# Optimization experiments

Measured on AMD Instinct MI355X. Metric: run time of the kernel, lower is better.

Reference implementation:

```python
import jax, jax.numpy as jnp
import numpy as np

N0, N1, N2 = 120000, 30000, 6000   # node frontier sizes per hop
E0, E1 = 480000, 96000             # sampled edges per layer (~fanout 16)
D = 128                            # in_channels == hidden_size
R = 8                              # num_relations
NB = 4                             # num_bases
ETOT = 3000000                     # global edge count (edge_type_all)


def setup_inputs() -> dict:
    key = jax.random.key(0)
    ks = jax.random.split(key, 24)
    s = 1.0 / np.sqrt(D)
    f32 = jnp.float32
    inp = {
        "x": jax.random.normal(ks[0], (N0, D), dtype=f32),
        "src0": jax.random.randint(ks[1], (E0,), 0, N0),
        "dst0": jax.random.randint(ks[2], (E0,), 0, N1),
        "e_id0": jax.random.randint(ks[3], (E0,), 0, ETOT),
        "src1": jax.random.randint(ks[4], (E1,), 0, N1),
        "dst1": jax.random.randint(ks[5], (E1,), 0, N2),
        "e_id1": jax.random.randint(ks[6], (E1,), 0, ETOT),
        "edge_type_all": jax.random.randint(ks[7], (ETOT,), 0, R),
        # pre_layer: linear + relu
        "pre_W": jax.random.normal(ks[8], (D, D), dtype=f32) * s,
        "pre_b": jnp.zeros((D,), f32),
        # RGCNConv layer 0 (basis decomposition)
        "basis0": jax.random.normal(ks[9], (NB, D, D), dtype=f32) * s,
        "comp0": jax.random.normal(ks[10], (R, NB), dtype=f32) * (1.0 / np.sqrt(NB)),
        "root0": jax.random.normal(ks[11], (D, D), dtype=f32) * s,
        "bias0": jnp.zeros((D,), f32),
        "g0": jnp.ones((D,), f32),
        "be0": jnp.zeros((D,), f32),
        # RGCNConv layer 1
        "basis1": jax.random.normal(ks[12], (NB, D, D), dtype=f32) * s,
        "comp1": jax.random.normal(ks[13], (R, NB), dtype=f32) * (1.0 / np.sqrt(NB)),
        "root1": jax.random.normal(ks[14], (D, D), dtype=f32) * s,
        "bias1": jnp.zeros((D,), f32),
        "g1": jnp.ones((D,), f32),
        "be1": jnp.zeros((D,), f32),
        # post_layer: single linear
        "post_W": jax.random.normal(ks[15], (D, D), dtype=f32) * s,
        "post_b": jnp.zeros((D,), f32),
    }
    return inp


def _layernorm(x, g, b, eps=1e-5):
    mu = jnp.mean(x, axis=-1, keepdims=True)
    var = jnp.mean(jnp.square(x - mu), axis=-1, keepdims=True)
    return (x - mu) * jax.lax.rsqrt(var + eps) * g + b


def _rgcn_conv(x, n_dst, src, dst, etype, basis, comp, root, bias):
    # Bipartite RGCNConv with basis decomposition and mean aggregation.
    # Since messages W[r] @ x[src] are linear, aggregate per relation first
    # (segment_sum of raw features), then apply the relation weight once.
    x_t = x[:n_dst]                                    # [n_dst, D]
    out = x_t @ root + bias                            # root/self transform
    W = jnp.einsum('rb,bio->rio', comp, basis)         # [R, D, D]
    x_j = x[src]                                       # [E, D] gather
    deg = jax.ops.segment_sum(jnp.ones(src.shape[0], x.dtype), dst,
                              num_segments=n_dst)      # mean over all relations
    agg = jnp.zeros((n_dst, W.shape[-1]), x.dtype)
    for r in range(W.shape[0]):                        # R=8 structurally distinct
        m = (etype == r).astype(x.dtype)[:, None]
        s_r = jax.ops.segment_sum(x_j * m, dst, num_segments=n_dst)
        agg = agg + s_r @ W[r]
    return out + agg / jnp.maximum(deg, 1.0)[:, None]


def reference(x, src0, dst0, e_id0, src1, dst1, e_id1, edge_type_all,
              pre_W, pre_b, basis0, comp0, root0, bias0, g0, be0,
              basis1, comp1, root1, bias1, g1, be1, post_W, post_b):
    # pre_layer: linear + relu (GeneralMultiLayer, final_act=True)
    h = jax.nn.relu(x @ pre_W + pre_b)
    # layer 0: edge-type gather -> relational conv -> norm -> act (eval: no dropout)
    h = _rgcn_conv(h, N1, src0, dst0, edge_type_all[e_id0],
                   basis0, comp0, root0, bias0)
    h = jax.nn.relu(_layernorm(h, g0, be0))
    # layer 1
    h = _rgcn_conv(h, N2, src1, dst1, edge_type_all[e_id1],
                   basis1, comp1, root1, bias1)
    h = jax.nn.relu(_layernorm(h, g1, be1))
    # post_layer: single linear MLP
    return h @ post_W + post_b
```

## Files before the change

### kernel.cpp

```cpp
#include <hip/hip_runtime.h>
#include <cstdint>

#define DD 128
#define CAP 64
#define ESB 128
#define E0C 480000
#define E1C 96000
#define N0C 120000
#define N1C 30000
#define N2C 6000

typedef unsigned short u16;
typedef __attribute__((ext_vector_type(8))) short bf16x8;
typedef __attribute__((ext_vector_type(16))) float f32x16;

__device__ __forceinline__ u16 f2b(float f) {
    union { float f; unsigned u; } a; a.f = f;
    unsigned r = (a.u + 0x7fffu + ((a.u >> 16) & 1u)) >> 16;
    return (u16)r;
}
__device__ __forceinline__ float b2f(u16 u) {
    union { unsigned u; float f; } a; a.u = ((unsigned)u) << 16;
    return a.f;
}

struct WtJob { const float* src[12]; };
__global__ __launch_bounds__(256) void prep_kernel(
    WtJob job, u16* __restrict__ dst, int* __restrict__ cnt0, int* __restrict__ cnt1)
{
    int gtid = blockIdx.x * 256 + threadIdx.x;
    for (int i = gtid; i < N1C + N2C; i += 256 * 256) {
        if (i < N1C) cnt0[i] = 0; else cnt1[i - N1C] = 0;
    }
    if (blockIdx.x >= 192) return;
    __shared__ float tile[32][33];
    int m = blockIdx.x >> 4;
    int t4 = blockIdx.x & 15;
    int tr = (t4 >> 2) * 32;
    int tc = (t4 & 3) * 32;
    int lx = threadIdx.x & 31, ly = threadIdx.x >> 5;
    #pragma unroll
    for (int yy = 0; yy < 32; yy += 8)
        tile[ly + yy][lx] = job.src[m][(tr + ly + yy) * DD + tc + lx];
    __syncthreads();
    int tid = threadIdx.x;
    if (tid < 128) {
        int nl = tid >> 2, kch = tid & 3;
        int k = tr + kch * 8, n = tc + nl;
        int kc = k >> 4, half = (k >> 3) & 1;
        int t = n >> 5, l31 = n & 31;
        bf16x8 pk;
        #pragma unroll
        for (int j = 0; j < 8; ++j) pk[j] = (short)f2b(tile[kch * 8 + j][nl]);
        *(bf16x8*)(dst + (size_t)m * 16384 + kc * 2048 + t * 512 + half * 256 + l31 * 8) = pk;
    }
}

__global__ __launch_bounds__(256) void pre_fill_kernel(
    const float* __restrict__ x,
    const int* __restrict__ src0, const int* __restrict__ dst0, const int* __restrict__ eid0,
    const int* __restrict__ src1, const int* __restrict__ dst1, const int* __restrict__ eid1,
    const int* __restrict__ etype,
    int* __restrict__ cnt0, int* __restrict__ cnt1,
    int* __restrict__ ep0, int* __restrict__ ep1,
    const u16* __restrict__ Wr, const float* __restrict__ bias,
    u16* __restrict__ h0)
{
    if (blockIdx.x < ESB) {
        const int STR = ESB * 256;
        int gtid = blockIdx.x * 256 + threadIdx.x;
        int e = gtid;
        for (; e + 3 * STR < E0C + E1C; e += 4 * STR) {
            int d[4], eidv[4], s[4], r[4], pos[4];
            bool L0[4];
            #pragma unroll
            for (int u = 0; u < 4; ++u) {
                int idx = e + u * STR;
                L0[u] = idx < E0C;
                int ee = L0[u] ? idx : idx - E0C;
                d[u]    = L0[u] ? dst0[ee] : dst1[ee];
                eidv[u] = L0[u] ? eid0[ee] : eid1[ee];
                s[u]    = L0[u] ? src0[ee] : src1[ee];
            }
            #pragma unroll
            for (int u = 0; u < 4; ++u) r[u] = etype[eidv[u]];
            #pragma unroll
            for (int u = 0; u < 4; ++u)
                pos[u] = atomicAdd(L0[u] ? &cnt0[d[u]] : &cnt1[d[u]], 1);
            #pragma unroll
            for (int u = 0; u < 4; ++u) {
                if (pos[u] < CAP) {
                    int* ep = L0[u] ? ep0 : ep1;
                    ep[(size_t)d[u] * CAP + pos[u]] = s[u] | (r[u] << 28);
                }
            }
        }
        for (; e < E0C + E1C; e += STR) {
            bool L0 = e < E0C;
            int ee = L0 ? e : e - E0C;
            int d   = L0 ? dst0[ee] : dst1[ee];
            int eid = L0 ? eid0[ee] : eid1[ee];
            int s   = L0 ? src0[ee] : src1[ee];
            int r = etype[eid];
            int pos = atomicAdd(L0 ? &cnt0[d] : &cnt1[d], 1);
            if (pos < CAP) (L0 ? ep0 : ep1)[(size_t)d * CAP + pos] = s | (r << 28);
        }
        return;
    }

    int bid = blockIdx.x - ESB;
    int wave = threadIdx.x >> 6;
    int lane = threadIdx.x & 63;
    int l31 = lane & 31, half = lane >> 5;
    int m0 = (bid * 4 + wave) * 32;
    if (m0 >= N0C) return;
    int arow = m0 + l31;
    bool rv = arow < N0C;

    const float* Aq = x + (size_t)arow * DD;
    float4 st[16];
    if (rv) {
        #pragma unroll
        for (int c = 0; c < 16; ++c)
            st[c] = *(const float4*)(Aq + ((c >> 1) * 16 + half * 8) + (c & 1) * 4);
    } else {
        #pragma unroll
        for (int c = 0; c < 16; ++c) st[c] = make_float4(0.f, 0.f, 0.f, 0.f);
    }
    f32x16 accs[4];
    #pragma unroll
    for (int t = 0; t < 4; ++t)
        #pragma unroll
        for (int i = 0; i < 16; ++i) accs[t][i] = 0.f;
    #pragma unroll
    for (int kc = 0; kc < 8; ++kc) {
        bf16x8 bfr[4];
        #pragma unroll
        for (int t = 0; t < 4; ++t)
            bfr[t] = *(const bf16x8*)(Wr + (size_t)((kc * 4 + t) * 64 + lane) * 8);
        float4 u0 = st[2 * kc], u1 = st[2 * kc + 1];
        bf16x8 af;
        af[0] = (short)f2b(u0.x); af[1] = (short)f2b(u0.y);
        af[2] = (short)f2b(u0.z); af[3] = (short)f2b(u0.w);
        af[4] = (short)f2b(u1.x); af[5] = (short)f2b(u1.y);
        af[6] = (short)f2b(u1.z); af[7] = (short)f2b(u1.w);
        #pragma unroll
        for (int t = 0; t < 4; ++t)
            accs[t] = __builtin_amdgcn_mfma_f32_32x32x16_bf16(af, bfr[t], accs[t], 0, 0, 0);
    }
    float bb[4];
    #pragma unroll
    for (int t = 0; t < 4; ++t) bb[t] = bias[t * 32 + l31];
    #pragma unroll
    for (int reg = 0; reg < 16; ++reg) {
        int rl = (reg & 3) + 8 * (reg >> 2) + 4 * half;
        int row = m0 + rl;
        if (row < N0C) {
            #pragma unroll
            for (int t = 0; t < 4; ++t)
                h0[(size_t)row * DD + t * 32 + l31] =
                    f2b(fmaxf(accs[t][reg] + bb[t], 0.f));
        }
    }
}

__global__ __launch_bounds__(256) void agg_kernel(
    const u16* __restrict__ h, const int* __restrict__ cnt,
    const int* __restrict__ ep, const float* __restrict__ comp,
    u16* __restrict__ T, int ndst)
{
    __shared__ float4 cmp4[8];
    if (threadIdx.x < 8) cmp4[threadIdx.x] = ((const float4*)comp)[threadIdx.x];
    __syncthreads();
    int row = blockIdx.x * 4 + (threadIdx.x >> 6);
    if (row >= ndst) return;
    int lane = threadIdx.x & 63;
    int n = cnt[row];
    int end = n < CAP ? n : CAP;
    const int* erow = ep + (size_t)row * CAP;
    float a0[4] = {0.f, 0.f, 0.f, 0.f};
    float a1[4] = {0.f, 0.f, 0.f, 0.f};
    int j = 0;
    for (; j + 16 <= end; j += 16) {
        int vv[16]; unsigned gg[16];
        #pragma unroll
        for (int u = 0; u < 16; ++u) vv[u] = erow[j + u];
        #pragma unroll
        for (int u = 0; u < 16; ++u)
            gg[u] = *(const unsigned*)(h + (size_t)(vv[u] & 0x0FFFFFFF) * DD + 2 * lane);
        #pragma unroll
        for (int u = 0; u < 16; ++u) {
            float4 c = cmp4[vv[u] >> 28];
            float x0 = b2f((u16)(gg[u] & 0xffffu));
            float x1 = b2f((u16)(gg[u] >> 16));
            a0[0] = fmaf(c.x, x0, a0[0]); a1[0] = fmaf(c.x, x1, a1[0]);
            a0[1] = fmaf(c.y, x0, a0[1]); a1[1] = fmaf(c.y, x1, a1[1]);
            a0[2] = fmaf(c.z, x0, a0[2]); a1[2] = fmaf(c.z, x1, a1[2]);
            a0[3] = fmaf(c.w, x0, a0[3]); a1[3] = fmaf(c.w, x1, a1[3]);
        }
    }
    for (; j + 4 <= end; j += 4) {
        int vv[4]; unsigned gg[4];
        #pragma unroll
        for (int u = 0; u < 4; ++u) vv[u] = erow[j + u];
        #pragma unroll
        for (int u = 0; u < 4; ++u)
            gg[u] = *(const unsigned*)(h + (size_t)(vv[u] & 0x0FFFFFFF) * DD + 2 * lane);
        #pragma unroll
        for (int u = 0; u < 4; ++u) {
            float4 c = cmp4[vv[u] >> 28];
            float x0 = b2f((u16)(gg[u] & 0xffffu));
            float x1 = b2f((u16)(gg[u] >> 16));
            a0[0] = fmaf(c.x, x0, a0[0]); a1[0] = fmaf(c.x, x1, a1[0]);
            a0[1] = fmaf(c.y, x0, a0[1]); a1[1] = fmaf(c.y, x1, a1[1]);
            a0[2] = fmaf(c.z, x0, a0[2]); a1[2] = fmaf(c.z, x1, a1[2]);
            a0[3] = fmaf(c.w, x0, a0[3]); a1[3] = fmaf(c.w, x1, a1[3]);
        }
    }
    for (; j < end; ++j) {
        int v = erow[j];
        unsigned g = *(const unsigned*)(h + (size_t)(v & 0x0FFFFFFF) * DD + 2 * lane);
        float4 c = cmp4[v >> 28];
        float x0 = b2f((u16)(g & 0xffffu));
        float x1 = b2f((u16)(g >> 16));
        a0[0] = fmaf(c.x, x0, a0[0]); a1[0] = fmaf(c.x, x1, a1[0]);
        a0[1] = fmaf(c.y, x0, a0[1]); a1[1] = fmaf(c.y, x1, a1[1]);
        a0[2] = fmaf(c.z, x0, a0[2]); a1[2] = fmaf(c.z, x1, a1[2]);
        a0[3] = fmaf(c.w, x0, a0[3]); a1[3] = fmaf(c.w, x1, a1[3]);
    }
    float inv = 1.f / fmaxf((float)n, 1.f);
    #pragma unroll
    for (int b = 0; b < 4; ++b) {
        unsigned pk = (unsigned)f2b(a0[b] * inv) | ((unsigned)f2b(a1[b] * inv) << 16);
        *(unsigned*)(T + ((size_t)b * ndst + row) * DD + 2 * lane) = pk;
    }
}

template<bool OBF16, bool LN>
__global__ __launch_bounds__(64) void mfma_gemm(
    const u16* __restrict__ Ap, int nplanes, const u16* __restrict__ Ar,
    const u16* __restrict__ Wp, const u16* __restrict__ Wr,
    const float* __restrict__ bias, const float* __restrict__ gw,
    const float* __restrict__ bw, void* __restrict__ Cv, int nrows)
{
    int lane = threadIdx.x & 63;
    int l31 = lane & 31, half = lane >> 5;
    int m0 = blockIdx.x * 32;
    int arow = m0 + l31;
    bool rv = arow < nrows;
    f32x16 acc[4];
    #pragma unroll
    for (int t = 0; t < 4; ++t)
        #pragma unroll
        for (int i = 0; i < 16; ++i) acc[t][i] = 0.f;

    bf16x8 A0[8], A1[8];
    {
        const u16* Ainit = (nplanes == 0) ? Ar : Ap;
        if (rv) {
            #pragma unroll
            for (int c = 0; c < 8; ++c)
                A0[c] = *(const bf16x8*)(Ainit + (size_t)arow * DD + c * 16 + half * 8);
        } else {
            #pragma unroll
            for (int c = 0; c < 8; ++c) A0[c] = (bf16x8){0,0,0,0,0,0,0,0};
        }
    }
    for (int p = 0; p <= nplanes; ++p) {
        const u16* Wsel = (p == nplanes) ? Wr : Wp + p * 16384;
        if (p < nplanes) {
            const u16* An = (p + 1 == nplanes) ? Ar : Ap + (size_t)(p + 1) * nrows * DD;
            if (rv) {
                #pragma unroll
                for (int c = 0; c < 8; ++c)
                    A1[c] = *(const bf16x8*)(An + (size_t)arow * DD + c * 16 + half * 8);
            } else {
                #pragma unroll
                for (int c = 0; c < 8; ++c) A1[c] = (bf16x8){0,0,0,0,0,0,0,0};
            }
        }
        #pragma unroll
        for (int kc = 0; kc < 8; ++kc) {
            bf16x8 bfr[4];
            #pragma unroll
            for (int t = 0; t < 4; ++t)
                bfr[t] = *(const bf16x8*)(Wsel + (size_t)((kc * 4 + t) * 64 + lane) * 8);
            #pragma unroll
            for (int t = 0; t < 4; ++t)
                acc[t] = __builtin_amdgcn_mfma_f32_32x32x16_bf16(A0[kc], bfr[t], acc[t], 0, 0, 0);
        }
        if (p < nplanes) {
            #pragma unroll
            for (int c = 0; c < 8; ++c) A0[c] = A1[c];
        }
    }

    float bb[4];
    #pragma unroll
    for (int t = 0; t < 4; ++t) bb[t] = bias[t * 32 + l31];
    float gg[4], ww[4];
    if (LN) {
        #pragma unroll
        for (int t = 0; t < 4; ++t) { gg[t] = gw[t * 32 + l31]; ww[t] = bw[t * 32 + l31]; }
    }

    #pragma unroll
    for (int reg = 0; reg < 16; ++reg) {
        int rl = (reg & 3) + 8 * (reg >> 2) + 4 * half;
        int row = m0 + rl;
        float v[4];
        #pragma unroll
        for (int t = 0; t < 4; ++t) v[t] = acc[t][reg] + bb[t];
        if (LN) {
            float s1 = 0.f, s2 = 0.f;
            #pragma unroll
            for (int t = 0; t < 4; ++t) { s1 += v[t]; s2 += v[t] * v[t]; }
            #pragma unroll
            for (int o = 1; o < 32; o <<= 1) {
                s1 += __shfl_xor(s1, o);
                s2 += __shfl_xor(s2, o);
            }
            float mu = s1 * (1.f / 128.f);
            float var = s2 * (1.f / 128.f) - mu * mu;
            float rstd = rsqrtf(fmaxf(var, 0.f) + 1e-5f);
            #pragma unroll
            for (int t = 0; t < 4; ++t)
                v[t] = fmaxf((v[t] - mu) * rstd * gg[t] + ww[t], 0.f);
        }
        if (row < nrows) {
            #pragma unroll
            for (int t = 0; t < 4; ++t) {
                if (OBF16) ((u16*)Cv)[(size_t)row * DD + t * 32 + l31] = f2b(v[t]);
                else       ((float*)Cv)[(size_t)row * DD + t * 32 + l31] = v[t];
            }
        }
    }
}

extern "C" void kernel_launch(void* const* d_in, const int* in_sizes, int n_in,
                              void* d_out, int out_size, void* d_ws, size_t ws_size,
                              hipStream_t stream)
{
    const float* x     = (const float*)d_in[0];
    const int* src0    = (const int*)d_in[1];
    const int* dst0    = (const int*)d_in[2];
    const int* eid0    = (const int*)d_in[3];
    const int* src1    = (const int*)d_in[4];
    const int* dst1    = (const int*)d_in[5];
    const int* eid1    = (const int*)d_in[6];
    const int* etype   = (const int*)d_in[7];
    const float* preW  = (const float*)d_in[8];
    const float* preb  = (const float*)d_in[9];
    const float* basis0 = (const float*)d_in[10];
    const float* comp0  = (const float*)d_in[11];
    const float* root0  = (const float*)d_in[12];
    const float* bias0  = (const float*)d_in[13];
    const float* g0    = (const float*)d_in[14];
    const float* be0   = (const float*)d_in[15];
    const float* basis1 = (const float*)d_in[16];
    const float* comp1  = (const float*)d_in[17];
    const float* root1  = (const float*)d_in[18];
    const float* bias1  = (const float*)d_in[19];
    const float* g1    = (const float*)d_in[20];
    const float* be1   = (const float*)d_in[21];
    const float* postW = (const float*)d_in[22];
    const float* postb = (const float*)d_in[23];
    float* out = (float*)d_out;

    char* ws = (char*)d_ws;
    size_t o = 0;
    auto alloc = [&](size_t bytes) { char* p = ws + o; o += (bytes + 255) & ~(size_t)255; return p; };
    u16* h0   = (u16*)alloc((size_t)N0C * DD * 2);
    u16* T0   = (u16*)alloc((size_t)4 * N1C * DD * 2);
    u16* h1   = (u16*)alloc((size_t)N1C * DD * 2);
    u16* T1   = (u16*)alloc((size_t)4 * N2C * DD * 2);
    u16* h2   = (u16*)alloc((size_t)N2C * DD * 2);
    u16* wt   = (u16*)alloc((size_t)12 * 16384 * 2);
    int* cnt0 = (int*)alloc((size_t)N1C * 4);
    int* cnt1 = (int*)alloc((size_t)N2C * 4);
    int* ep0  = (int*)alloc((size_t)N1C * CAP * 4);
    int* ep1  = (int*)alloc((size_t)N2C * CAP * 4);

    WtJob job;
    job.src[0] = preW;
    for (int b = 0; b < 4; ++b) job.src[1 + b] = basis0 + (size_t)b * 16384;
    job.src[5] = root0;
    for (int b = 0; b < 4; ++b) job.src[6 + b] = basis1 + (size_t)b * 16384;
    job.src[10] = root1;
    job.src[11] = postW;

    prep_kernel<<<256, 256, 0, stream>>>(job, wt, cnt0, cnt1);
    pre_fill_kernel<<<ESB + (N0C + 127) / 128, 256, 0, stream>>>(
        x, src0, dst0, eid0, src1, dst1, eid1, etype,
        cnt0, cnt1, ep0, ep1, wt + 0 * 16384, preb, h0);
    agg_kernel<<<(N1C + 3) / 4, 256, 0, stream>>>(h0, cnt0, ep0, comp0, T0, N1C);
    mfma_gemm<true, true><<<(N1C + 31) / 32, 64, 0, stream>>>(
        T0, 4, h0, wt + 1 * 16384, wt + 5 * 16384, bias0, g0, be0, h1, N1C);
    agg_kernel<<<(N2C + 3) / 4, 256, 0, stream>>>(h1, cnt1, ep1, comp1, T1, N2C);
    mfma_gemm<true, true><<<(N2C + 31) / 32, 64, 0, stream>>>(
        T1, 4, h1, wt + 6 * 16384, wt + 10 * 16384, bias1, g1, be1, h2, N2C);
    mfma_gemm<false, false><<<(N2C + 31) / 32, 64, 0, stream>>>(
        nullptr, 0, h2, nullptr, wt + 11 * 16384, postb, nullptr, nullptr, out, N2C);
}
```

Baseline: 293.8 us.

## Split fused edge-fill/pre-GEMM kernel into separate one-edge-per-thread fill and GEMM kernels

Replaces the combined kernel, where 128 blocks grid-strided over all edges while the remaining blocks ran the pre-layer GEMM, with two kernels. The fill kernel now uses one thread per edge across 2250 blocks, and the GEMM becomes its own launch. The aim is to stop a few long-running edge-scatter blocks from forming a tail under the GEMM blocks. The cost is an extra kernel launch and the loss of concurrent overlap between the atomic scatter and the GEMM.

```diff
diff --git a/kernel.cpp b/kernel.cpp
--- a/kernel.cpp
+++ b/kernel.cpp
@@ -3,7 +3,6 @@
 
 #define DD 128
 #define CAP 64
-#define ESB 128
 #define E0C 480000
 #define E1C 96000
 #define N0C 120000
@@ -56,63 +55,34 @@
     }
 }
 
-__global__ __launch_bounds__(256) void pre_fill_kernel(
-    const float* __restrict__ x,
+__global__ __launch_bounds__(256) void fill_kernel(
     const int* __restrict__ src0, const int* __restrict__ dst0, const int* __restrict__ eid0,
     const int* __restrict__ src1, const int* __restrict__ dst1, const int* __restrict__ eid1,
     const int* __restrict__ etype,
     int* __restrict__ cnt0, int* __restrict__ cnt1,
-    int* __restrict__ ep0, int* __restrict__ ep1,
-    const u16* __restrict__ Wr, const float* __restrict__ bias,
-    u16* __restrict__ h0)
-{
-    if (blockIdx.x < ESB) {
-        const int STR = ESB * 256;
-        int gtid = blockIdx.x * 256 + threadIdx.x;
-        int e = gtid;
-        for (; e + 3 * STR < E0C + E1C; e += 4 * STR) {
-            int d[4], eidv[4], s[4], r[4], pos[4];
-            bool L0[4];
-            #pragma unroll
-            for (int u = 0; u < 4; ++u) {
-                int idx = e + u * STR;
-                L0[u] = idx < E0C;
-                int ee = L0[u] ? idx : idx - E0C;
-                d[u]    = L0[u] ? dst0[ee] : dst1[ee];
-                eidv[u] = L0[u] ? eid0[ee] : eid1[ee];
-                s[u]    = L0[u] ? src0[ee] : src1[ee];
-            }
-            #pragma unroll
-            for (int u = 0; u < 4; ++u) r[u] = etype[eidv[u]];
-            #pragma unroll
-            for (int u = 0; u < 4; ++u)
-                pos[u] = atomicAdd(L0[u] ? &cnt0[d[u]] : &cnt1[d[u]], 1);
-            #pragma unroll
-            for (int u = 0; u < 4; ++u) {
-                if (pos[u] < CAP) {
-                    int* ep = L0[u] ? ep0 : ep1;
-                    ep[(size_t)d[u] * CAP + pos[u]] = s[u] | (r[u] << 28);
-                }
-            }
-        }
-        for (; e < E0C + E1C; e += STR) {
-            bool L0 = e < E0C;
-            int ee = L0 ? e : e - E0C;
-            int d   = L0 ? dst0[ee] : dst1[ee];
-            int eid = L0 ? eid0[ee] : eid1[ee];
-            int s   = L0 ? src0[ee] : src1[ee];
-            int r = etype[eid];
-            int pos = atomicAdd(L0 ? &cnt0[d] : &cnt1[d], 1);
-            if (pos < CAP) (L0 ? ep0 : ep1)[(size_t)d * CAP + pos] = s | (r << 28);
-        }
-        return;
-    }
-
-    int bid = blockIdx.x - ESB;
+    int* __restrict__ ep0, int* __restrict__ ep1)
+{
+    int idx = blockIdx.x * 256 + threadIdx.x;
+    bool L0 = idx < E0C;
+    int ee = L0 ? idx : idx - E0C;
+    if (ee >= (L0 ? E0C : E1C)) return;
+    int s   = L0 ? src0[ee] : src1[ee];
+    int d   = L0 ? dst0[ee] : dst1[ee];
+    int eid = L0 ? eid0[ee] : eid1[ee];
+    int r = etype[eid];
+    int pos = atomicAdd((L0 ? cnt0 : cnt1) + d, 1);
+    if (pos < CAP)
+        (L0 ? ep0 : ep1)[(size_t)d * CAP + pos] = s | (r << 28);
+}
+
+__global__ __launch_bounds__(256) void pre_gemm_kernel(
+    const float* __restrict__ x, const u16* __restrict__ Wr,
+    const float* __restrict__ bias, u16* __restrict__ h0)
+{
     int wave = threadIdx.x >> 6;
     int lane = threadIdx.x & 63;
     int l31 = lane & 31, half = lane >> 5;
-    int m0 = (bid * 4 + wave) * 32;
+    int m0 = (blockIdx.x * 4 + wave) * 32;
     if (m0 >= N0C) return;
     int arow = m0 + l31;
     bool rv = arow < N0C;
@@ -390,9 +360,10 @@
     job.src[11] = postW;
 
     prep_kernel<<<256, 256, 0, stream>>>(job, wt, cnt0, cnt1);
-    pre_fill_kernel<<<ESB + (N0C + 127) / 128, 256, 0, stream>>>(
-        x, src0, dst0, eid0, src1, dst1, eid1, etype,
-        cnt0, cnt1, ep0, ep1, wt + 0 * 16384, preb, h0);
+    fill_kernel<<<(E0C + E1C) / 256, 256, 0, stream>>>(
+        src0, dst0, eid0, src1, dst1, eid1, etype, cnt0, cnt1, ep0, ep1);
+    pre_gemm_kernel<<<(N0C + 127) / 128, 256, 0, stream>>>(
+        x, wt + 0 * 16384, preb, h0);
     agg_kernel<<<(N1C + 3) / 4, 256, 0, stream>>>(h0, cnt0, ep0, comp0, T0, N1C);
     mfma_gemm<true, true><<<(N1C + 31) / 32, 64, 0, stream>>>(
         T0, 4, h0, wt + 1 * 16384, wt + 5 * 16384, bias0, g0, be0, h1, N1C);
```

Measured after the change: 300.8 us. 2.4% more time.
